# Optimization experiments

Measured on AMD Instinct MI355X. Metric: run time of the kernel, lower is better.

The kernel has to match this reference:

```python
import jax, jax.numpy as jnp
import numpy as np

INPUT_SZ = 1024
HIDDEN_SZ = 1024

def setup_inputs() -> dict:
    key = jax.random.key(0)
    k1, k2, k3 = jax.random.split(key, 3)
    x = jax.random.normal(k1, (64, 512, INPUT_SZ), dtype=jnp.float32)
    # nn.Linear(input_sz+hidden_sz, hidden_sz): weight [hidden, input+hidden], bias [hidden]
    bound = 1.0 / np.sqrt(INPUT_SZ + HIDDEN_SZ)
    W = jax.random.uniform(k2, (HIDDEN_SZ, INPUT_SZ + HIDDEN_SZ), dtype=jnp.float32, minval=-bound, maxval=bound)
    b = jax.random.uniform(k3, (HIDDEN_SZ,), dtype=jnp.float32, minval=-bound, maxval=bound)
    return {"x": x, "W": W, "b": b}

def reference(x, W, b):
    # Split the concat-linear into two contractions: [x_t, h_t] @ W.T = x_t @ Wx.T + h_t @ Wh.T
    Wx = W[:, :INPUT_SZ]   # [H, I]
    Wh = W[:, INPUT_SZ:]   # [H, H]
    B = x.shape[0]
    # Precompute the input projection for all timesteps in one big GEMM.
    xp = jnp.einsum('bti,hi->bth', x, Wx) + b  # [B, T, H]
    h0 = jnp.zeros((B, HIDDEN_SZ), dtype=x.dtype)

    def step(h, xp_t):
        h_new = jnp.tanh(xp_t + h @ Wh.T)
        return h_new, h_new

    _, hs = jax.lax.scan(step, h0, jnp.swapaxes(xp, 0, 1))  # hs: [T, B, H]
    return jnp.swapaxes(hs, 0, 1)  # [B, T, H]
```

## Files before the change

### kernel.cpp

```cpp
#include <hip/hip_runtime.h>


typedef unsigned short u16;
typedef unsigned u32;
typedef unsigned long long u64;
typedef __attribute__((ext_vector_type(4))) float f32x4;
typedef __attribute__((ext_vector_type(8))) short bf16x8;
typedef __attribute__((ext_vector_type(4))) u32 u32x4;

__device__ __forceinline__ u16 f2bf(float f) {
  unsigned u = __builtin_bit_cast(unsigned, f);
  unsigned r = (u + 0x7fffu + ((u >> 16) & 1u)) >> 16;
  return (u16)r;
}

__device__ __forceinline__ u16 f2bf_par(float f, unsigned bit) {
  unsigned rt = __builtin_bit_cast(unsigned, f) >> 16;
  return (u16)(((rt & 1u) == bit) ? rt : rt + 1u);
}

__device__ __forceinline__ float fast_tanh(float x) {
  float e = __expf(2.0f * x);
  return 1.0f - 2.0f / (e + 1.0f);
}

__device__ __forceinline__ void async_cp16(u16* lds, const u16* g) {
  __builtin_amdgcn_global_load_lds(
      (const __attribute__((address_space(1))) unsigned int*)g,
      (__attribute__((address_space(3))) unsigned int*)lds, 16, 0, 0);
}


__global__ __launch_bounds__(256) void conv_x_kernel(const float* __restrict__ in,
                                                     u16* __restrict__ outb) {
  const size_t i = (size_t)blockIdx.x * 256 + threadIdx.x;
  const float4* p = (const float4*)(in + (i << 3));
  float4 a = p[0], b = p[1];
  bf16x8 v;
  v[0] = (short)f2bf(a.x); v[1] = (short)f2bf(a.y);
  v[2] = (short)f2bf(a.z); v[3] = (short)f2bf(a.w);
  v[4] = (short)f2bf(b.x); v[5] = (short)f2bf(b.y);
  v[6] = (short)f2bf(b.z); v[7] = (short)f2bf(b.w);
  *(bf16x8*)(outb + (i << 3)) = v;
}

__global__ __launch_bounds__(256) void conv_w_kernel(const float* __restrict__ W,
                                                     u16* __restrict__ Wx,
                                                     u16* __restrict__ Wh) {
  const int i = blockIdx.x * 256 + threadIdx.x;
  const int j = i >> 8;
  const int c = (i & 255) << 3;
  const float4* p = (const float4*)(W + (size_t)j * 2048 + c);
  float4 a = p[0], b = p[1];
  bf16x8 v;
  v[0] = (short)f2bf(a.x); v[1] = (short)f2bf(a.y);
  v[2] = (short)f2bf(a.z); v[3] = (short)f2bf(a.w);
  v[4] = (short)f2bf(b.x); v[5] = (short)f2bf(b.y);
  v[6] = (short)f2bf(b.z); v[7] = (short)f2bf(b.w);
  u16* dst = (c < 1024) ? (Wx + (size_t)j * 1024 + c)
                        : (Wh + (size_t)j * 1024 + (c - 1024));
  *(bf16x8*)dst = v;
}


__global__ __launch_bounds__(256, 2) void gemm_xp(const u16* __restrict__ A,
                                                  const u16* __restrict__ B,
                                                  const float* __restrict__ bias,
                                                  float* __restrict__ C) {
  const int bid = blockIdx.x;
  const int swz = (bid & 7) * 256 + (bid >> 3);
  const int m0 = (swz >> 3) << 7;
  const int n0 = (swz & 7) << 7;
  const int tid = threadIdx.x;
  const int lane = tid & 63;
  const int wv = tid >> 6;
  const int mw = (wv >> 1) << 6;
  const int nw = (wv & 1) << 6;

  __shared__ __align__(16) u16 Alds[128 * 32];
  __shared__ __align__(16) u16 Blds[128 * 32];

  f32x4 acc[4][4] = {};

  for (int kt = 0; kt < 32; ++kt) {
    const int k0 = kt << 5;
#pragma unroll
    for (int i = 0; i < 2; ++i) {
      const int off = (i << 11) + (tid << 3);
      const int row = off >> 5;
      const int col = off & 31;
      async_cp16(&Alds[off], A + (size_t)(m0 + row) * 1024 + k0 + col);
      async_cp16(&Blds[off], B + (size_t)(n0 + row) * 1024 + k0 + col);
    }
    __syncthreads();
    bf16x8 af[4], bf[4];
#pragma unroll
    for (int mi = 0; mi < 4; ++mi)
      af[mi] = *(const bf16x8*)&Alds[((mw + (mi << 4) + (lane & 15)) << 5) +
                                     ((lane >> 4) << 3)];
#pragma unroll
    for (int ni = 0; ni < 4; ++ni)
      bf[ni] = *(const bf16x8*)&Blds[((nw + (ni << 4) + (lane & 15)) << 5) +
                                     ((lane >> 4) << 3)];
#pragma unroll
    for (int mi = 0; mi < 4; ++mi)
#pragma unroll
      for (int ni = 0; ni < 4; ++ni)
        acc[mi][ni] = __builtin_amdgcn_mfma_f32_16x16x32_bf16(
            af[mi], bf[ni], acc[mi][ni], 0, 0, 0);
    __syncthreads();
  }

  float bv[4];
#pragma unroll
  for (int ni = 0; ni < 4; ++ni)
    bv[ni] = bias[n0 + nw + (ni << 4) + (lane & 15)];
#pragma unroll
  for (int mi = 0; mi < 4; ++mi) {
#pragma unroll
    for (int r = 0; r < 4; ++r) {
      const int row = m0 + mw + (mi << 4) + ((lane >> 4) << 2) + r;
      float* cp = C + (size_t)row * 1024 + n0 + nw + (lane & 15);
#pragma unroll
      for (int ni = 0; ni < 4; ++ni) cp[ni << 4] = acc[mi][ni][r] + bv[ni];
    }
  }
}


__global__ __launch_bounds__(256) void rnn_scan(float* __restrict__ out,
                                                const u16* __restrict__ Wh,
                                                char* __restrict__ Hb) {
  const int wg = blockIdx.x;
  const int g = wg & 3;
  const int wloc = wg >> 2;
  const int tid = threadIdx.x;
  const int lane = tid & 63;
  const int wv = tid >> 6;
  const int l16 = lane & 15;
  const int lhi = lane >> 4;

  __shared__ __align__(16) f32x4 red[2][4][4][64];

  bf16x8 af[4][8];
  {
    const u16* wp =
        Wh + (size_t)((wloc << 6) + l16) * 1024 + (wv << 8) + (lhi << 3);
#pragma unroll
    for (int jt = 0; jt < 4; ++jt)
#pragma unroll
      for (int kk = 0; kk < 8; ++kk)
        af[jt][kk] = *(const bf16x8*)(wp + (jt << 14) + (kk << 5));
  }

  const int b = (g << 4) + l16;
  const int hread = (g << 15) + (((wv << 5) + lhi) << 8) + (l16 << 4);
  const int jq = (wloc << 4) + (wv << 2) + lhi;
  const int hwrite = (g << 15) + ((jq >> 1) << 8) + (l16 << 4) + ((jq & 1) << 3);
  const int j0 = jq << 2;
  float* pout = out + ((size_t)b << 19) + j0;

  f32x4 xpA = __builtin_nontemporal_load((const f32x4*)pout);
  f32x4 xpB = __builtin_nontemporal_load((const f32x4*)(pout + 1024));
  f32x4 hvP = {0.f, 0.f, 0.f, 0.f};

#pragma unroll 1
  for (int t = 0; t < 512; ++t) {
    f32x4 acc[4] = {};
    if (t > 0) {
      const u32 e = 1u + ((((u32)t - 1u) >> 1) & 1u);
      const char* Hs = Hb + (((t - 1) & 1) << 17) + hread;
      const char* Hs2 = Hs + 4096;
      u32x4 f0, f1, f2, f3, f4, f5, f6, f7;
      while (true) {
        asm volatile(
            "global_load_dwordx4 %0, %8, off sc0 sc1\n\t"
            "global_load_dwordx4 %1, %8, off offset:1024 sc0 sc1\n\t"
            "global_load_dwordx4 %2, %8, off offset:2048 sc0 sc1\n\t"
            "global_load_dwordx4 %3, %8, off offset:3072 sc0 sc1\n\t"
            "global_load_dwordx4 %4, %9, off sc0 sc1\n\t"
            "global_load_dwordx4 %5, %9, off offset:1024 sc0 sc1\n\t"
            "global_load_dwordx4 %6, %9, off offset:2048 sc0 sc1\n\t"
            "global_load_dwordx4 %7, %9, off offset:3072 sc0 sc1\n\t"
            "s_waitcnt vmcnt(0)"
            : "=&v"(f0), "=&v"(f1), "=&v"(f2), "=&v"(f3), "=&v"(f4),
              "=&v"(f5), "=&v"(f6), "=&v"(f7)
            : "v"(Hs), "v"(Hs2)
            : "memory");
        u32 ok = 1u;
#pragma unroll
        for (int d = 0; d < 4; ++d) {
          ok &= (u32)(((f0[d] & 1u) | (((f0[d] >> 16) & 1u) << 1)) == e);
          ok &= (u32)(((f1[d] & 1u) | (((f1[d] >> 16) & 1u) << 1)) == e);
          ok &= (u32)(((f2[d] & 1u) | (((f2[d] >> 16) & 1u) << 1)) == e);
          ok &= (u32)(((f3[d] & 1u) | (((f3[d] >> 16) & 1u) << 1)) == e);
          ok &= (u32)(((f4[d] & 1u) | (((f4[d] >> 16) & 1u) << 1)) == e);
          ok &= (u32)(((f5[d] & 1u) | (((f5[d] >> 16) & 1u) << 1)) == e);
          ok &= (u32)(((f6[d] & 1u) | (((f6[d] >> 16) & 1u) << 1)) == e);
          ok &= (u32)(((f7[d] & 1u) | (((f7[d] >> 16) & 1u) << 1)) == e);
        }
        if (__all((int)ok)) break;
      }
      __builtin_nontemporal_store(hvP,
                                  (f32x4*)(pout + ((size_t)(t - 1) << 10)));
      union { u32x4 u; bf16x8 v; } c[8];
      c[0].u = f0; c[1].u = f1; c[2].u = f2; c[3].u = f3;
      c[4].u = f4; c[5].u = f5; c[6].u = f6; c[7].u = f7;
#pragma unroll
      for (int kk = 0; kk < 8; ++kk)
#pragma unroll
        for (int jt = 0; jt < 4; ++jt)
          acc[jt] = __builtin_amdgcn_mfma_f32_16x16x32_bf16(af[jt][kk], c[kk].v,
                                                            acc[jt], 0, 0, 0);
    }

    const int rb = t & 1;
#pragma unroll
    for (int jt = 0; jt < 4; ++jt) red[rb][wv][jt][lane] = acc[jt];
    asm volatile("s_waitcnt lgkmcnt(0)\n\ts_barrier" ::: "memory");

    f32x4 s = red[rb][0][wv][lane];
#pragma unroll
    for (int w = 1; w < 4; ++w) s += red[rb][w][wv][lane];

    const f32x4 xp = (t & 1) ? xpB : xpA;
    const float h0 = fast_tanh(xp[0] + s[0]);
    const float h1 = fast_tanh(xp[1] + s[1]);
    const float h2 = fast_tanh(xp[2] + s[2]);
    const float h3 = fast_tanh(xp[3] + s[3]);

    const u32 code = 1u + (((u32)t >> 1) & 1u);
    const u32 c0b = code & 1u, c1b = (code >> 1) & 1u;
    const u64 pack = (u64)f2bf_par(h0, c0b) | ((u64)f2bf_par(h1, c1b) << 16) |
                     ((u64)f2bf_par(h2, c0b) << 32) |
                     ((u64)f2bf_par(h3, c1b) << 48);
    __hip_atomic_store((u64*)(Hb + ((t & 1) << 17) + hwrite), pack,
                       __ATOMIC_RELAXED, __HIP_MEMORY_SCOPE_AGENT);

    if (t + 2 < 512) {
      const f32x4* src = (const f32x4*)(pout + ((size_t)(t + 2) << 10));
      if (t & 1)
        xpB = __builtin_nontemporal_load(src);
      else
        xpA = __builtin_nontemporal_load(src);
    }
    hvP[0] = h0; hvP[1] = h1; hvP[2] = h2; hvP[3] = h3;
  }
  __builtin_nontemporal_store(hvP, (f32x4*)(pout + ((size_t)511 << 10)));
}


extern "C" void kernel_launch(void* const* d_in, const int* in_sizes, int n_in,
                              void* d_out, int out_size, void* d_ws,
                              size_t ws_size, hipStream_t stream) {
  const float* x = (const float*)d_in[0];
  const float* W = (const float*)d_in[1];
  const float* bias = (const float*)d_in[2];
  float* out = (float*)d_out;

  char* ws = (char*)d_ws;
  u16* xb = (u16*)ws;
  u16* Wxb = (u16*)(ws + 67108864);
  u16* Whb = (u16*)(ws + 69206016);
  char* Hbuf = (char*)(ws + 71303168);

  (void)hipMemsetAsync(Hbuf, 0, 262144, stream);
  conv_x_kernel<<<16384, 256, 0, stream>>>(x, xb);
  conv_w_kernel<<<1024, 256, 0, stream>>>(W, Wxb, Whb);
  gemm_xp<<<2048, 256, 0, stream>>>(xb, Wxb, bias, out);
  rnn_scan<<<64, 256, 0, stream>>>(out, Whb, Hbuf);
}
```

Before: 1.053 ms.

## Fuse input projection into the recurrent scan and overlap it with h polling

Removes the separate xp GEMM kernel. Each scan workgroup now keeps its Wx slice in registers and computes x_t @ Wx.T with MFMA inside the time loop. That MFMA work is issued between launching the h-buffer loads and checking their parity flags, so it fills the inter-block synchronisation wait, and the next step's x tile is prefetched into registers. This cuts a full-size fp32 write and read of xp and one launch, but doubles the weight registers per thread and adds per-step compute and x loads to the latency-bound serial loop.

```diff
diff --git a/kernel.cpp b/kernel.cpp
--- a/kernel.cpp
+++ b/kernel.cpp
@@ -63,73 +63,26 @@
 }
 
 
-__global__ __launch_bounds__(256, 2) void gemm_xp(const u16* __restrict__ A,
-                                                  const u16* __restrict__ B,
-                                                  const float* __restrict__ bias,
-                                                  float* __restrict__ C) {
-  const int bid = blockIdx.x;
-  const int swz = (bid & 7) * 256 + (bid >> 3);
-  const int m0 = (swz >> 3) << 7;
-  const int n0 = (swz & 7) << 7;
-  const int tid = threadIdx.x;
-  const int lane = tid & 63;
-  const int wv = tid >> 6;
-  const int mw = (wv >> 1) << 6;
-  const int nw = (wv & 1) << 6;
-
-  __shared__ __align__(16) u16 Alds[128 * 32];
-  __shared__ __align__(16) u16 Blds[128 * 32];
-
-  f32x4 acc[4][4] = {};
-
-  for (int kt = 0; kt < 32; ++kt) {
-    const int k0 = kt << 5;
-#pragma unroll
-    for (int i = 0; i < 2; ++i) {
-      const int off = (i << 11) + (tid << 3);
-      const int row = off >> 5;
-      const int col = off & 31;
-      async_cp16(&Alds[off], A + (size_t)(m0 + row) * 1024 + k0 + col);
-      async_cp16(&Blds[off], B + (size_t)(n0 + row) * 1024 + k0 + col);
-    }
-    __syncthreads();
-    bf16x8 af[4], bf[4];
-#pragma unroll
-    for (int mi = 0; mi < 4; ++mi)
-      af[mi] = *(const bf16x8*)&Alds[((mw + (mi << 4) + (lane & 15)) << 5) +
-                                     ((lane >> 4) << 3)];
-#pragma unroll
-    for (int ni = 0; ni < 4; ++ni)
-      bf[ni] = *(const bf16x8*)&Blds[((nw + (ni << 4) + (lane & 15)) << 5) +
-                                     ((lane >> 4) << 3)];
-#pragma unroll
-    for (int mi = 0; mi < 4; ++mi)
-#pragma unroll
-      for (int ni = 0; ni < 4; ++ni)
-        acc[mi][ni] = __builtin_amdgcn_mfma_f32_16x16x32_bf16(
-            af[mi], bf[ni], acc[mi][ni], 0, 0, 0);
-    __syncthreads();
+#define CHECK8(OKVAR)                                                       \
+  {                                                                         \
+    OKVAR = 1u;                                                             \
+    _Pragma("unroll") for (int d = 0; d < 4; ++d) {                         \
+      OKVAR &= (u32)(((f0[d] & 1u) | (((f0[d] >> 16) & 1u) << 1)) == e);    \
+      OKVAR &= (u32)(((f1[d] & 1u) | (((f1[d] >> 16) & 1u) << 1)) == e);    \
+      OKVAR &= (u32)(((f2[d] & 1u) | (((f2[d] >> 16) & 1u) << 1)) == e);    \
+      OKVAR &= (u32)(((f3[d] & 1u) | (((f3[d] >> 16) & 1u) << 1)) == e);    \
+      OKVAR &= (u32)(((f4[d] & 1u) | (((f4[d] >> 16) & 1u) << 1)) == e);    \
+      OKVAR &= (u32)(((f5[d] & 1u) | (((f5[d] >> 16) & 1u) << 1)) == e);    \
+      OKVAR &= (u32)(((f6[d] & 1u) | (((f6[d] >> 16) & 1u) << 1)) == e);    \
+      OKVAR &= (u32)(((f7[d] & 1u) | (((f7[d] >> 16) & 1u) << 1)) == e);    \
+    }                                                                       \
   }
-
-  float bv[4];
-#pragma unroll
-  for (int ni = 0; ni < 4; ++ni)
-    bv[ni] = bias[n0 + nw + (ni << 4) + (lane & 15)];
-#pragma unroll
-  for (int mi = 0; mi < 4; ++mi) {
-#pragma unroll
-    for (int r = 0; r < 4; ++r) {
-      const int row = m0 + mw + (mi << 4) + ((lane >> 4) << 2) + r;
-      float* cp = C + (size_t)row * 1024 + n0 + nw + (lane & 15);
-#pragma unroll
-      for (int ni = 0; ni < 4; ++ni) cp[ni << 4] = acc[mi][ni][r] + bv[ni];
-    }
-  }
-}
-
 
 __global__ __launch_bounds__(256) void rnn_scan(float* __restrict__ out,
                                                 const u16* __restrict__ Wh,
+                                                const u16* __restrict__ Wx,
+                                                const u16* __restrict__ xb,
+                                                const float* __restrict__ bias,
                                                 char* __restrict__ Hb) {
   const int wg = blockIdx.x;
   const int g = wg & 3;
@@ -142,15 +95,18 @@
 
   __shared__ __align__(16) f32x4 red[2][4][4][64];
 
-  bf16x8 af[4][8];
+  bf16x8 af[4][8], afx[4][8];
   {
-    const u16* wp =
-        Wh + (size_t)((wloc << 6) + l16) * 1024 + (wv << 8) + (lhi << 3);
+    const size_t roff = (size_t)((wloc << 6) + l16) * 1024 + (wv << 8) + (lhi << 3);
+    const u16* wp = Wh + roff;
+    const u16* wpx = Wx + roff;
 #pragma unroll
     for (int jt = 0; jt < 4; ++jt)
 #pragma unroll
-      for (int kk = 0; kk < 8; ++kk)
+      for (int kk = 0; kk < 8; ++kk) {
         af[jt][kk] = *(const bf16x8*)(wp + (jt << 14) + (kk << 5));
+        afx[jt][kk] = *(const bf16x8*)(wpx + (jt << 14) + (kk << 5));
+      }
   }
 
   const int b = (g << 4) + l16;
@@ -159,20 +115,61 @@
   const int hwrite = (g << 15) + ((jq >> 1) << 8) + (l16 << 4) + ((jq & 1) << 3);
   const int j0 = jq << 2;
   float* pout = out + ((size_t)b << 19) + j0;
-
-  f32x4 xpA = __builtin_nontemporal_load((const f32x4*)pout);
-  f32x4 xpB = __builtin_nontemporal_load((const f32x4*)(pout + 1024));
+  const u16* xbase = xb + ((size_t)b << 19) + (wv << 8) + (lhi << 3);
+  const f32x4 bv = *(const f32x4*)(bias + j0);
+
+  u32x4 xfCur[8], xfNext[8];
+#pragma unroll
+  for (int kk = 0; kk < 8; ++kk)
+    xfNext[kk] = *(const u32x4*)(xbase + (kk << 5));
+
   f32x4 hvP = {0.f, 0.f, 0.f, 0.f};
 
 #pragma unroll 1
   for (int t = 0; t < 512; ++t) {
+#pragma unroll
+    for (int kk = 0; kk < 8; ++kk) xfCur[kk] = xfNext[kk];
+
     f32x4 acc[4] = {};
+    const char* Hs = Hb + (((t - 1) & 1) << 17) + hread;
+    const char* Hs2 = Hs + 4096;
+    u32x4 f0, f1, f2, f3, f4, f5, f6, f7;
+
+    if (t > 0) {
+      asm volatile(
+          "global_load_dwordx4 %0, %8, off sc0 sc1\n\t"
+          "global_load_dwordx4 %1, %8, off offset:1024 sc0 sc1\n\t"
+          "global_load_dwordx4 %2, %8, off offset:2048 sc0 sc1\n\t"
+          "global_load_dwordx4 %3, %8, off offset:3072 sc0 sc1\n\t"
+          "global_load_dwordx4 %4, %9, off sc0 sc1\n\t"
+          "global_load_dwordx4 %5, %9, off offset:1024 sc0 sc1\n\t"
+          "global_load_dwordx4 %6, %9, off offset:2048 sc0 sc1\n\t"
+          "global_load_dwordx4 %7, %9, off offset:3072 sc0 sc1"
+          : "=&v"(f0), "=&v"(f1), "=&v"(f2), "=&v"(f3), "=&v"(f4),
+            "=&v"(f5), "=&v"(f6), "=&v"(f7)
+          : "v"(Hs), "v"(Hs2)
+          : "memory");
+    }
+
+    {
+      union { u32x4 u; bf16x8 v; } xu;
+#pragma unroll
+      for (int kk = 0; kk < 8; ++kk) {
+        xu.u = xfCur[kk];
+#pragma unroll
+        for (int jt = 0; jt < 4; ++jt)
+          acc[jt] = __builtin_amdgcn_mfma_f32_16x16x32_bf16(afx[jt][kk], xu.v,
+                                                            acc[jt], 0, 0, 0);
+      }
+    }
+
     if (t > 0) {
       const u32 e = 1u + ((((u32)t - 1u) >> 1) & 1u);
-      const char* Hs = Hb + (((t - 1) & 1) << 17) + hread;
-      const char* Hs2 = Hs + 4096;
-      u32x4 f0, f1, f2, f3, f4, f5, f6, f7;
-      while (true) {
+      asm volatile("s_waitcnt vmcnt(0)" ::: "memory");
+      __builtin_amdgcn_sched_barrier(0);
+      u32 ok;
+      CHECK8(ok)
+      while (!__all((int)ok)) {
         asm volatile(
             "global_load_dwordx4 %0, %8, off sc0 sc1\n\t"
             "global_load_dwordx4 %1, %8, off offset:1024 sc0 sc1\n\t"
@@ -187,19 +184,8 @@
               "=&v"(f5), "=&v"(f6), "=&v"(f7)
             : "v"(Hs), "v"(Hs2)
             : "memory");
-        u32 ok = 1u;
-#pragma unroll
-        for (int d = 0; d < 4; ++d) {
-          ok &= (u32)(((f0[d] & 1u) | (((f0[d] >> 16) & 1u) << 1)) == e);
-          ok &= (u32)(((f1[d] & 1u) | (((f1[d] >> 16) & 1u) << 1)) == e);
-          ok &= (u32)(((f2[d] & 1u) | (((f2[d] >> 16) & 1u) << 1)) == e);
-          ok &= (u32)(((f3[d] & 1u) | (((f3[d] >> 16) & 1u) << 1)) == e);
-          ok &= (u32)(((f4[d] & 1u) | (((f4[d] >> 16) & 1u) << 1)) == e);
-          ok &= (u32)(((f5[d] & 1u) | (((f5[d] >> 16) & 1u) << 1)) == e);
-          ok &= (u32)(((f6[d] & 1u) | (((f6[d] >> 16) & 1u) << 1)) == e);
-          ok &= (u32)(((f7[d] & 1u) | (((f7[d] >> 16) & 1u) << 1)) == e);
-        }
-        if (__all((int)ok)) break;
+        __builtin_amdgcn_sched_barrier(0);
+        CHECK8(ok)
       }
       __builtin_nontemporal_store(hvP,
                                   (f32x4*)(pout + ((size_t)(t - 1) << 10)));
@@ -214,6 +200,13 @@
                                                             acc[jt], 0, 0, 0);
     }
 
+    {
+      const u16* xnp = xbase + ((size_t)((t < 511) ? t + 1 : 511) << 10);
+#pragma unroll
+      for (int kk = 0; kk < 8; ++kk)
+        xfNext[kk] = *(const u32x4*)(xnp + (kk << 5));
+    }
+
     const int rb = t & 1;
 #pragma unroll
     for (int jt = 0; jt < 4; ++jt) red[rb][wv][jt][lane] = acc[jt];
@@ -223,11 +216,10 @@
 #pragma unroll
     for (int w = 1; w < 4; ++w) s += red[rb][w][wv][lane];
 
-    const f32x4 xp = (t & 1) ? xpB : xpA;
-    const float h0 = fast_tanh(xp[0] + s[0]);
-    const float h1 = fast_tanh(xp[1] + s[1]);
-    const float h2 = fast_tanh(xp[2] + s[2]);
-    const float h3 = fast_tanh(xp[3] + s[3]);
+    const float h0 = fast_tanh(s[0] + bv[0]);
+    const float h1 = fast_tanh(s[1] + bv[1]);
+    const float h2 = fast_tanh(s[2] + bv[2]);
+    const float h3 = fast_tanh(s[3] + bv[3]);
 
     const u32 code = 1u + (((u32)t >> 1) & 1u);
     const u32 c0b = code & 1u, c1b = (code >> 1) & 1u;
@@ -237,13 +229,6 @@
     __hip_atomic_store((u64*)(Hb + ((t & 1) << 17) + hwrite), pack,
                        __ATOMIC_RELAXED, __HIP_MEMORY_SCOPE_AGENT);
 
-    if (t + 2 < 512) {
-      const f32x4* src = (const f32x4*)(pout + ((size_t)(t + 2) << 10));
-      if (t & 1)
-        xpB = __builtin_nontemporal_load(src);
-      else
-        xpA = __builtin_nontemporal_load(src);
-    }
     hvP[0] = h0; hvP[1] = h1; hvP[2] = h2; hvP[3] = h3;
   }
   __builtin_nontemporal_store(hvP, (f32x4*)(pout + ((size_t)511 << 10)));
@@ -267,6 +252,5 @@
   (void)hipMemsetAsync(Hbuf, 0, 262144, stream);
   conv_x_kernel<<<16384, 256, 0, stream>>>(x, xb);
   conv_w_kernel<<<1024, 256, 0, stream>>>(W, Wxb, Whb);
-  gemm_xp<<<2048, 256, 0, stream>>>(xb, Wxb, bias, out);
-  rnn_scan<<<64, 256, 0, stream>>>(out, Whb, Hbuf);
-}
+  rnn_scan<<<64, 256, 0, stream>>>(out, Whb, Wxb, xb, bias, Hbuf);
+}
```

After: 1.487 ms. +41.2%, slower.

## Fuse input-projection GEMM into the RNN scan kernel with per-chunk readiness flags

Applied to the files above, without the earlier changes.

Merges the input-projection GEMM and the recurrent scan into one launch. Blocks 0-63 run the scan, and the rest compute xp tiles ordered by time quarter, bumping a per-quarter counter when they finish. The scan waits on each quarter's counter before reading that slice of xp, so the scan can start while later GEMM tiles are still running. It also converts x to bf16 inside the GEMM's LDS load, which removes the separate conversion kernel and its 64MB intermediate buffer. The risks are the cost of the spin-wait polling, the slower fp32 load path for A without async copy, and possible deadlock if the 64 scan blocks are not all co-resident.

```diff
diff --git a/kernel.cpp b/kernel.cpp
--- a/kernel.cpp
+++ b/kernel.cpp
@@ -30,19 +30,17 @@
       (__attribute__((address_space(3))) unsigned int*)lds, 16, 0, 0);
 }
 
-
-__global__ __launch_bounds__(256) void conv_x_kernel(const float* __restrict__ in,
-                                                     u16* __restrict__ outb) {
-  const size_t i = (size_t)blockIdx.x * 256 + threadIdx.x;
-  const float4* p = (const float4*)(in + (i << 3));
-  float4 a = p[0], b = p[1];
-  bf16x8 v;
-  v[0] = (short)f2bf(a.x); v[1] = (short)f2bf(a.y);
-  v[2] = (short)f2bf(a.z); v[3] = (short)f2bf(a.w);
-  v[4] = (short)f2bf(b.x); v[5] = (short)f2bf(b.y);
-  v[6] = (short)f2bf(b.z); v[7] = (short)f2bf(b.w);
-  *(bf16x8*)(outb + (i << 3)) = v;
-}
+__device__ __forceinline__ f32x4 ld_xp16(const float* p) {
+  f32x4 v;
+  asm volatile("global_load_dwordx4 %0, %1, off sc0 sc1\n\ts_waitcnt vmcnt(0)"
+               : "=v"(v) : "v"(p) : "memory");
+  return v;
+}
+__device__ __forceinline__ void st_f32(float* p, float v) {
+  asm volatile("global_store_dword %0, %1, off sc0 sc1" ::"v"(p), "v"(v)
+               : "memory");
+}
+
 
 __global__ __launch_bounds__(256) void conv_w_kernel(const float* __restrict__ W,
                                                      u16* __restrict__ Wx,
@@ -63,84 +61,98 @@
 }
 
 
-__global__ __launch_bounds__(256, 2) void gemm_xp(const u16* __restrict__ A,
-                                                  const u16* __restrict__ B,
-                                                  const float* __restrict__ bias,
-                                                  float* __restrict__ C) {
-  const int bid = blockIdx.x;
-  const int swz = (bid & 7) * 256 + (bid >> 3);
-  const int m0 = (swz >> 3) << 7;
-  const int n0 = (swz & 7) << 7;
-  const int tid = threadIdx.x;
-  const int lane = tid & 63;
-  const int wv = tid >> 6;
-  const int mw = (wv >> 1) << 6;
-  const int nw = (wv & 1) << 6;
-
+__global__ __launch_bounds__(256) void rnn_fused(float* __restrict__ out,
+                                                 const u16* __restrict__ Wh,
+                                                 const u16* __restrict__ Wx,
+                                                 const float* __restrict__ x,
+                                                 const float* __restrict__ bias,
+                                                 char* __restrict__ Hb,
+                                                 u32* __restrict__ wm) {
+  __shared__ __align__(16) f32x4 red[2][4][4][64];
   __shared__ __align__(16) u16 Alds[128 * 32];
   __shared__ __align__(16) u16 Blds[128 * 32];
 
-  f32x4 acc[4][4] = {};
-
-  for (int kt = 0; kt < 32; ++kt) {
-    const int k0 = kt << 5;
-#pragma unroll
-    for (int i = 0; i < 2; ++i) {
-      const int off = (i << 11) + (tid << 3);
-      const int row = off >> 5;
-      const int col = off & 31;
-      async_cp16(&Alds[off], A + (size_t)(m0 + row) * 1024 + k0 + col);
-      async_cp16(&Blds[off], B + (size_t)(n0 + row) * 1024 + k0 + col);
-    }
-    __syncthreads();
-    bf16x8 af[4], bf[4];
-#pragma unroll
-    for (int mi = 0; mi < 4; ++mi)
-      af[mi] = *(const bf16x8*)&Alds[((mw + (mi << 4) + (lane & 15)) << 5) +
-                                     ((lane >> 4) << 3)];
-#pragma unroll
-    for (int ni = 0; ni < 4; ++ni)
-      bf[ni] = *(const bf16x8*)&Blds[((nw + (ni << 4) + (lane & 15)) << 5) +
-                                     ((lane >> 4) << 3)];
-#pragma unroll
-    for (int mi = 0; mi < 4; ++mi)
-#pragma unroll
-      for (int ni = 0; ni < 4; ++ni)
-        acc[mi][ni] = __builtin_amdgcn_mfma_f32_16x16x32_bf16(
-            af[mi], bf[ni], acc[mi][ni], 0, 0, 0);
-    __syncthreads();
-  }
-
-  float bv[4];
-#pragma unroll
-  for (int ni = 0; ni < 4; ++ni)
-    bv[ni] = bias[n0 + nw + (ni << 4) + (lane & 15)];
-#pragma unroll
-  for (int mi = 0; mi < 4; ++mi) {
-#pragma unroll
-    for (int r = 0; r < 4; ++r) {
-      const int row = m0 + mw + (mi << 4) + ((lane >> 4) << 2) + r;
-      float* cp = C + (size_t)row * 1024 + n0 + nw + (lane & 15);
-#pragma unroll
-      for (int ni = 0; ni < 4; ++ni) cp[ni << 4] = acc[mi][ni][r] + bv[ni];
-    }
-  }
-}
-
-
-__global__ __launch_bounds__(256) void rnn_scan(float* __restrict__ out,
-                                                const u16* __restrict__ Wh,
-                                                char* __restrict__ Hb) {
-  const int wg = blockIdx.x;
-  const int g = wg & 3;
-  const int wloc = wg >> 2;
+  const int bid = blockIdx.x;
   const int tid = threadIdx.x;
   const int lane = tid & 63;
   const int wv = tid >> 6;
   const int l16 = lane & 15;
   const int lhi = lane >> 4;
 
-  __shared__ __align__(16) f32x4 red[2][4][4][64];
+  if (bid >= 64) {
+    const int q = bid - 64;
+    const int d = q >> 3;
+    const int nq = q & 7;
+    const int bq = d & 63;
+    const int tq = d >> 6;
+    const int m0 = (bq << 9) + (tq << 7);
+    const int n0 = nq << 7;
+    const int mw = (wv >> 1) << 6;
+    const int nw = (wv & 1) << 6;
+
+    f32x4 acc[4][4] = {};
+
+    for (int kt = 0; kt < 32; ++kt) {
+      const int k0 = kt << 5;
+#pragma unroll
+      for (int i = 0; i < 2; ++i) {
+        const int off = (i << 11) + (tid << 3);
+        const int row = off >> 5;
+        const int col = off & 31;
+        const float* ap = x + (size_t)(m0 + row) * 1024 + k0 + col;
+        float4 a0 = *(const float4*)ap;
+        float4 a1 = *(const float4*)(ap + 4);
+        bf16x8 av;
+        av[0] = (short)f2bf(a0.x); av[1] = (short)f2bf(a0.y);
+        av[2] = (short)f2bf(a0.z); av[3] = (short)f2bf(a0.w);
+        av[4] = (short)f2bf(a1.x); av[5] = (short)f2bf(a1.y);
+        av[6] = (short)f2bf(a1.z); av[7] = (short)f2bf(a1.w);
+        *(bf16x8*)&Alds[off] = av;
+        async_cp16(&Blds[off], Wx + (size_t)(n0 + row) * 1024 + k0 + col);
+      }
+      __syncthreads();
+      bf16x8 af[4], bf[4];
+#pragma unroll
+      for (int mi = 0; mi < 4; ++mi)
+        af[mi] = *(const bf16x8*)&Alds[((mw + (mi << 4) + l16) << 5) +
+                                       (lhi << 3)];
+#pragma unroll
+      for (int ni = 0; ni < 4; ++ni)
+        bf[ni] = *(const bf16x8*)&Blds[((nw + (ni << 4) + l16) << 5) +
+                                       (lhi << 3)];
+#pragma unroll
+      for (int mi = 0; mi < 4; ++mi)
+#pragma unroll
+        for (int ni = 0; ni < 4; ++ni)
+          acc[mi][ni] = __builtin_amdgcn_mfma_f32_16x16x32_bf16(
+              af[mi], bf[ni], acc[mi][ni], 0, 0, 0);
+      __syncthreads();
+    }
+
+    float bv[4];
+#pragma unroll
+    for (int ni = 0; ni < 4; ++ni) bv[ni] = bias[n0 + nw + (ni << 4) + l16];
+#pragma unroll
+    for (int mi = 0; mi < 4; ++mi) {
+#pragma unroll
+      for (int r = 0; r < 4; ++r) {
+        const int row = m0 + mw + (mi << 4) + (lhi << 2) + r;
+        float* cp = out + (size_t)row * 1024 + n0 + nw + l16;
+#pragma unroll
+        for (int ni = 0; ni < 4; ++ni)
+          st_f32(cp + (ni << 4), acc[mi][ni][r] + bv[ni]);
+      }
+    }
+    asm volatile("s_waitcnt vmcnt(0)" ::: "memory");
+    __syncthreads();
+    if (tid == 0)
+      __hip_atomic_fetch_add(wm + tq, 1u, __ATOMIC_RELAXED,
+                             __HIP_MEMORY_SCOPE_AGENT);
+    return;
+  }
+
+  const int g = bid & 3;
+  const int wloc = bid >> 2;
 
   bf16x8 af[4][8];
   {
@@ -160,9 +172,16 @@
   const int j0 = jq << 2;
   float* pout = out + ((size_t)b << 19) + j0;
 
-  f32x4 xpA = __builtin_nontemporal_load((const f32x4*)pout);
-  f32x4 xpB = __builtin_nontemporal_load((const f32x4*)(pout + 1024));
+  {
+    u32 w;
+    do {
+      w = __hip_atomic_load(wm, __ATOMIC_RELAXED, __HIP_MEMORY_SCOPE_AGENT);
+    } while (w != 512u);
+  }
+  f32x4 xpA = ld_xp16(pout);
+  f32x4 xpB = ld_xp16(pout + 1024);
   f32x4 hvP = {0.f, 0.f, 0.f, 0.f};
+  int ready_tq = 0;
 
 #pragma unroll 1
   for (int t = 0; t < 512; ++t) {
@@ -189,15 +208,15 @@
             : "memory");
         u32 ok = 1u;
 #pragma unroll
-        for (int d = 0; d < 4; ++d) {
-          ok &= (u32)(((f0[d] & 1u) | (((f0[d] >> 16) & 1u) << 1)) == e);
-          ok &= (u32)(((f1[d] & 1u) | (((f1[d] >> 16) & 1u) << 1)) == e);
-          ok &= (u32)(((f2[d] & 1u) | (((f2[d] >> 16) & 1u) << 1)) == e);
-          ok &= (u32)(((f3[d] & 1u) | (((f3[d] >> 16) & 1u) << 1)) == e);
-          ok &= (u32)(((f4[d] & 1u) | (((f4[d] >> 16) & 1u) << 1)) == e);
-          ok &= (u32)(((f5[d] & 1u) | (((f5[d] >> 16) & 1u) << 1)) == e);
-          ok &= (u32)(((f6[d] & 1u) | (((f6[d] >> 16) & 1u) << 1)) == e);
-          ok &= (u32)(((f7[d] & 1u) | (((f7[d] >> 16) & 1u) << 1)) == e);
+        for (int dd = 0; dd < 4; ++dd) {
+          ok &= (u32)(((f0[dd] & 1u) | (((f0[dd] >> 16) & 1u) << 1)) == e);
+          ok &= (u32)(((f1[dd] & 1u) | (((f1[dd] >> 16) & 1u) << 1)) == e);
+          ok &= (u32)(((f2[dd] & 1u) | (((f2[dd] >> 16) & 1u) << 1)) == e);
+          ok &= (u32)(((f3[dd] & 1u) | (((f3[dd] >> 16) & 1u) << 1)) == e);
+          ok &= (u32)(((f4[dd] & 1u) | (((f4[dd] >> 16) & 1u) << 1)) == e);
+          ok &= (u32)(((f5[dd] & 1u) | (((f5[dd] >> 16) & 1u) << 1)) == e);
+          ok &= (u32)(((f6[dd] & 1u) | (((f6[dd] >> 16) & 1u) << 1)) == e);
+          ok &= (u32)(((f7[dd] & 1u) | (((f7[dd] >> 16) & 1u) << 1)) == e);
         }
         if (__all((int)ok)) break;
       }
@@ -238,11 +257,20 @@
                        __ATOMIC_RELAXED, __HIP_MEMORY_SCOPE_AGENT);
 
     if (t + 2 < 512) {
-      const f32x4* src = (const f32x4*)(pout + ((size_t)(t + 2) << 10));
+      const int tq2 = (t + 2) >> 7;
+      if (tq2 > ready_tq) {
+        u32 w;
+        do {
+          w = __hip_atomic_load(wm + tq2, __ATOMIC_RELAXED,
+                                __HIP_MEMORY_SCOPE_AGENT);
+        } while (w != 512u);
+        ready_tq = tq2;
+      }
+      const f32x4 v = ld_xp16(pout + ((size_t)(t + 2) << 10));
       if (t & 1)
-        xpB = __builtin_nontemporal_load(src);
+        xpB = v;
       else
-        xpA = __builtin_nontemporal_load(src);
+        xpA = v;
     }
     hvP[0] = h0; hvP[1] = h1; hvP[2] = h2; hvP[3] = h3;
   }
@@ -259,14 +287,12 @@
   float* out = (float*)d_out;
 
   char* ws = (char*)d_ws;
-  u16* xb = (u16*)ws;
-  u16* Wxb = (u16*)(ws + 67108864);
-  u16* Whb = (u16*)(ws + 69206016);
-  char* Hbuf = (char*)(ws + 71303168);
-
-  (void)hipMemsetAsync(Hbuf, 0, 262144, stream);
-  conv_x_kernel<<<16384, 256, 0, stream>>>(x, xb);
+  u16* Wxb = (u16*)ws;
+  u16* Whb = (u16*)(ws + 2097152);
+  char* Hbuf = (char*)(ws + 4194304);
+  u32* wm = (u32*)(ws + 4456448);
+
+  (void)hipMemsetAsync(Hbuf, 0, 262144 + 64, stream);
   conv_w_kernel<<<1024, 256, 0, stream>>>(W, Wxb, Whb);
-  gemm_xp<<<2048, 256, 0, stream>>>(xb, Wxb, bias, out);
-  rnn_scan<<<64, 256, 0, stream>>>(out, Whb, Hbuf);
-}
+  rnn_fused<<<2112, 256, 0, stream>>>(out, Whb, Wxb, x, bias, Hbuf, wm);
+}
```

Measured after the change: 1.115 ms. 5.9% more time.

## Give each wave full-K hidden reduction, drop LDS cross-wave reduction and barrier

Applied to the files above, without the earlier changes.

Each wave now covers the full 1024-wide K dimension for its own 16 output columns, so the split-K LDS reduction and per-step workgroup barrier go away. Every wave loads the whole previous hidden state for its batch group (32 dwordx4 loads instead of 8). Weights are no longer held in registers; they are re-read from global memory (cache) inside the MFMA loop each step. The poll checks fewer flag elements per load and adds s_sleep between failed polls. The trade is removing intra-block synchronisation against four times the hidden-state traffic and weight reloads on the serial critical path.

```diff
diff --git a/kernel.cpp b/kernel.cpp
--- a/kernel.cpp
+++ b/kernel.cpp
@@ -128,6 +128,28 @@
 }
 
 
+#define PB4(F0, F1, F2, F3, BASE)                                         \
+  asm volatile("global_load_dwordx4 %0, %4, off sc0 sc1\n\t"              \
+               "global_load_dwordx4 %1, %4, off offset:1024 sc0 sc1\n\t"  \
+               "global_load_dwordx4 %2, %4, off offset:2048 sc0 sc1\n\t"  \
+               "global_load_dwordx4 %3, %4, off offset:3072 sc0 sc1"      \
+               : "=&v"(F0), "=&v"(F1), "=&v"(F2), "=&v"(F3)               \
+               : "v"(BASE)                                                \
+               : "memory");
+
+#define CK(V)                                                              \
+  ok &= (u32)((((V)[0] & 1u) | ((((V)[0] >> 16) & 1u) << 1)) == e);        \
+  ok &= (u32)((((V)[2] & 1u) | ((((V)[2] >> 16) & 1u) << 1)) == e);
+
+#define MF(IDX, Q)                                                         \
+  {                                                                        \
+    union { u32x4 u; bf16x8 v; } u_;                                      \
+    u_.u = Q;                                                              \
+    const bf16x8 a_ = *(const bf16x8*)(wp + ((IDX) << 5));                 \
+    acc[(IDX) & 3] = __builtin_amdgcn_mfma_f32_16x16x32_bf16(              \
+        a_, u_.v, acc[(IDX) & 3], 0, 0, 0);                                \
+  }
+
 __global__ __launch_bounds__(256) void rnn_scan(float* __restrict__ out,
                                                 const u16* __restrict__ Wh,
                                                 char* __restrict__ Hb) {
@@ -140,21 +162,11 @@
   const int l16 = lane & 15;
   const int lhi = lane >> 4;
 
-  __shared__ __align__(16) f32x4 red[2][4][4][64];
-
-  bf16x8 af[4][8];
-  {
-    const u16* wp =
-        Wh + (size_t)((wloc << 6) + l16) * 1024 + (wv << 8) + (lhi << 3);
-#pragma unroll
-    for (int jt = 0; jt < 4; ++jt)
-#pragma unroll
-      for (int kk = 0; kk < 8; ++kk)
-        af[jt][kk] = *(const bf16x8*)(wp + (jt << 14) + (kk << 5));
-  }
+  const int j0w = (wloc << 6) + (wv << 4);
+  const u16* wp = Wh + (size_t)(j0w + l16) * 1024 + (lhi << 3);
 
   const int b = (g << 4) + l16;
-  const int hread = (g << 15) + (((wv << 5) + lhi) << 8) + (l16 << 4);
+  const int hread = (g << 15) + (lhi << 8) + (l16 << 4);
   const int jq = (wloc << 4) + (wv << 2) + lhi;
   const int hwrite = (g << 15) + ((jq >> 1) << 8) + (l16 << 4) + ((jq & 1) << 3);
   const int j0 = jq << 2;
@@ -170,59 +182,40 @@
     if (t > 0) {
       const u32 e = 1u + ((((u32)t - 1u) >> 1) & 1u);
       const char* Hs = Hb + (((t - 1) & 1) << 17) + hread;
-      const char* Hs2 = Hs + 4096;
-      u32x4 f0, f1, f2, f3, f4, f5, f6, f7;
+      u32x4 q0, q1, q2, q3, q4, q5, q6, q7, q8, q9, q10, q11, q12, q13, q14,
+          q15, q16, q17, q18, q19, q20, q21, q22, q23, q24, q25, q26, q27,
+          q28, q29, q30, q31;
       while (true) {
-        asm volatile(
-            "global_load_dwordx4 %0, %8, off sc0 sc1\n\t"
-            "global_load_dwordx4 %1, %8, off offset:1024 sc0 sc1\n\t"
-            "global_load_dwordx4 %2, %8, off offset:2048 sc0 sc1\n\t"
-            "global_load_dwordx4 %3, %8, off offset:3072 sc0 sc1\n\t"
-            "global_load_dwordx4 %4, %9, off sc0 sc1\n\t"
-            "global_load_dwordx4 %5, %9, off offset:1024 sc0 sc1\n\t"
-            "global_load_dwordx4 %6, %9, off offset:2048 sc0 sc1\n\t"
-            "global_load_dwordx4 %7, %9, off offset:3072 sc0 sc1\n\t"
-            "s_waitcnt vmcnt(0)"
-            : "=&v"(f0), "=&v"(f1), "=&v"(f2), "=&v"(f3), "=&v"(f4),
-              "=&v"(f5), "=&v"(f6), "=&v"(f7)
-            : "v"(Hs), "v"(Hs2)
-            : "memory");
+        PB4(q0, q1, q2, q3, Hs)
+        PB4(q4, q5, q6, q7, Hs + 4096)
+        PB4(q8, q9, q10, q11, Hs + 8192)
+        PB4(q12, q13, q14, q15, Hs + 12288)
+        PB4(q16, q17, q18, q19, Hs + 16384)
+        PB4(q20, q21, q22, q23, Hs + 20480)
+        PB4(q24, q25, q26, q27, Hs + 24576)
+        PB4(q28, q29, q30, q31, Hs + 28672)
+        asm volatile("s_waitcnt vmcnt(0)" ::: "memory");
         u32 ok = 1u;
-#pragma unroll
-        for (int d = 0; d < 4; ++d) {
-          ok &= (u32)(((f0[d] & 1u) | (((f0[d] >> 16) & 1u) << 1)) == e);
-          ok &= (u32)(((f1[d] & 1u) | (((f1[d] >> 16) & 1u) << 1)) == e);
-          ok &= (u32)(((f2[d] & 1u) | (((f2[d] >> 16) & 1u) << 1)) == e);
-          ok &= (u32)(((f3[d] & 1u) | (((f3[d] >> 16) & 1u) << 1)) == e);
-          ok &= (u32)(((f4[d] & 1u) | (((f4[d] >> 16) & 1u) << 1)) == e);
-          ok &= (u32)(((f5[d] & 1u) | (((f5[d] >> 16) & 1u) << 1)) == e);
-          ok &= (u32)(((f6[d] & 1u) | (((f6[d] >> 16) & 1u) << 1)) == e);
-          ok &= (u32)(((f7[d] & 1u) | (((f7[d] >> 16) & 1u) << 1)) == e);
-        }
+        CK(q0) CK(q1) CK(q2) CK(q3) CK(q4) CK(q5) CK(q6) CK(q7)
+        CK(q8) CK(q9) CK(q10) CK(q11) CK(q12) CK(q13) CK(q14) CK(q15)
+        CK(q16) CK(q17) CK(q18) CK(q19) CK(q20) CK(q21) CK(q22) CK(q23)
+        CK(q24) CK(q25) CK(q26) CK(q27) CK(q28) CK(q29) CK(q30) CK(q31)
         if (__all((int)ok)) break;
+        __builtin_amdgcn_s_sleep(1);
       }
       __builtin_nontemporal_store(hvP,
                                   (f32x4*)(pout + ((size_t)(t - 1) << 10)));
-      union { u32x4 u; bf16x8 v; } c[8];
-      c[0].u = f0; c[1].u = f1; c[2].u = f2; c[3].u = f3;
-      c[4].u = f4; c[5].u = f5; c[6].u = f6; c[7].u = f7;
-#pragma unroll
-      for (int kk = 0; kk < 8; ++kk)
-#pragma unroll
-        for (int jt = 0; jt < 4; ++jt)
-          acc[jt] = __builtin_amdgcn_mfma_f32_16x16x32_bf16(af[jt][kk], c[kk].v,
-                                                            acc[jt], 0, 0, 0);
-    }
-
-    const int rb = t & 1;
-#pragma unroll
-    for (int jt = 0; jt < 4; ++jt) red[rb][wv][jt][lane] = acc[jt];
-    asm volatile("s_waitcnt lgkmcnt(0)\n\ts_barrier" ::: "memory");
-
-    f32x4 s = red[rb][0][wv][lane];
-#pragma unroll
-    for (int w = 1; w < 4; ++w) s += red[rb][w][wv][lane];
-
+      MF(0, q0) MF(1, q1) MF(2, q2) MF(3, q3)
+      MF(4, q4) MF(5, q5) MF(6, q6) MF(7, q7)
+      MF(8, q8) MF(9, q9) MF(10, q10) MF(11, q11)
+      MF(12, q12) MF(13, q13) MF(14, q14) MF(15, q15)
+      MF(16, q16) MF(17, q17) MF(18, q18) MF(19, q19)
+      MF(20, q20) MF(21, q21) MF(22, q22) MF(23, q23)
+      MF(24, q24) MF(25, q25) MF(26, q26) MF(27, q27)
+      MF(28, q28) MF(29, q29) MF(30, q30) MF(31, q31)
+    }
+
+    const f32x4 s = (acc[0] + acc[1]) + (acc[2] + acc[3]);
     const f32x4 xp = (t & 1) ? xpB : xpA;
     const float h0 = fast_tanh(xp[0] + s[0]);
     const float h1 = fast_tanh(xp[1] + s[1]);
```

Result: slower. 3.506 ms (+233.0%).
